# Optimization experiments

Hardware: AMD Instinct MI355X
Metric: run time of the kernel (lower is better)

The kernel has to match this reference:

```python
import jax, jax.numpy as jnp
import numpy as np

D_MODEL = 768
NHEAD = 12
HEAD_DIM = D_MODEL // NHEAD


def setup_inputs() -> dict:
    key = jax.random.key(0)
    ks = jax.random.split(key, 5)
    B, S = 1, 4096
    x = jax.random.normal(ks[0], (B, S, D_MODEL), dtype=jnp.float32)
    # Linear params (stored as [in, out] so y = x @ W + b)
    s_in = 1.0 / np.sqrt(D_MODEL)
    W_qkv = jax.random.uniform(ks[1], (D_MODEL, 3 * D_MODEL), minval=-s_in, maxval=s_in, dtype=jnp.float32)
    b_qkv = jax.random.uniform(ks[2], (3 * D_MODEL,), minval=-s_in, maxval=s_in, dtype=jnp.float32)
    W_o = jax.random.uniform(ks[3], (D_MODEL, D_MODEL), minval=-s_in, maxval=s_in, dtype=jnp.float32)
    b_o = jax.random.uniform(ks[4], (D_MODEL,), minval=-s_in, maxval=s_in, dtype=jnp.float32)
    return {"x": x, "W_qkv": W_qkv, "b_qkv": b_qkv, "W_o": W_o, "b_o": b_o}


def reference(x, W_qkv, b_qkv, W_o, b_o):
    B, S, _ = x.shape
    qkv = x @ W_qkv + b_qkv                      # [B,S,3D]
    qkv = qkv.reshape(B, S, 3, NHEAD, HEAD_DIM)
    q, k, v = qkv[:, :, 0], qkv[:, :, 1], qkv[:, :, 2]   # [B,S,H,hd]
    scale = D_MODEL ** (-0.5)                    # NOTE: d_model, not head_dim
    scores = jnp.einsum('bqhd,bkhd->bhqk', q, k) * scale
    attn = jax.nn.softmax(scores, axis=-1)
    out = jnp.einsum('bhqk,bkhd->bqhd', attn, v) * HEAD_DIM  # custom post-softmax rescale
    out = out.reshape(B, S, D_MODEL)
    return out @ W_o + b_o
```

## Files before the change

kernel.cpp:

```cpp
#include <hip/hip_runtime.h>
#include <stdint.h>
#include <math.h>

typedef unsigned short u16;
typedef __attribute__((ext_vector_type(8))) __bf16 bf16x8;
typedef __attribute__((ext_vector_type(4))) float f32x4;
typedef __attribute__((ext_vector_type(16))) float f32x16;
typedef __attribute__((ext_vector_type(4))) short short4v;
typedef __attribute__((ext_vector_type(4))) float float4v;
typedef __attribute__((ext_vector_type(2))) uint32_t u32x2;
typedef __attribute__((ext_vector_type(4))) uint32_t u32x4;

#define SEQ 4096
#define DM 768
#define NH 12

__device__ __forceinline__ u16 f2b(float f) {
  uint32_t u = __float_as_uint(f);
  uint32_t r = (u + 0x7fffu + ((u >> 16) & 1u)) >> 16;
  return (u16)r;
}

__device__ __forceinline__ uint32_t cvtpk(float lo, float hi) {
  uint32_t r;
  asm("v_cvt_pk_bf16_f32 %0, %1, %2" : "=v"(r) : "v"(lo), "v"(hi));
  return r;
}

__device__ __forceinline__ void gload16(const void* g, void* l) {
  __builtin_amdgcn_global_load_lds(
      (const __attribute__((address_space(1))) void*)g,
      (__attribute__((address_space(3))) void*)l, 16, 0, 0);
}

__device__ __forceinline__ f32x4 mfma16(bf16x8 a, bf16x8 b, f32x4 c) {
  return __builtin_amdgcn_mfma_f32_16x16x32_bf16(a, b, c, 0, 0, 0);
}

__device__ __forceinline__ f32x16 mfma32(bf16x8 a, bf16x8 b, f32x16 c) {
  return __builtin_amdgcn_mfma_f32_32x32x16_bf16(a, b, c, 0, 0, 0);
}

__device__ __forceinline__ float pexp2(float x) {
  return fmaf(fmaf(fmaf(0.0571709f, x, 0.249989f), x, 0.6927303f), x, 0.9987737f);
}

__global__ __launch_bounds__(256) void k_conv(const float* __restrict__ in,
                                              u16* __restrict__ out) {
  int i = blockIdx.x * 256 + threadIdx.x;
  float4v v = ((const float4v*)in)[i];
  short4v o;
  o.x = (short)f2b(v.x);
  o.y = (short)f2b(v.y);
  o.z = (short)f2b(v.z);
  o.w = (short)f2b(v.w);
  ((short4v*)out)[i] = o;
}

__global__ __launch_bounds__(256) void k_transconv(const float* __restrict__ in,
                                                   u16* __restrict__ out,
                                                   int R, int C) {
  __shared__ float tile[32][33];
  int tx = threadIdx.x & 31, ty = threadIdx.x >> 5;
  int r0 = blockIdx.y * 32, c0 = blockIdx.x * 32;
#pragma unroll
  for (int k = 0; k < 4; ++k)
    tile[ty + 8 * k][tx] = in[(size_t)(r0 + ty + 8 * k) * C + c0 + tx];
  __syncthreads();
#pragma unroll
  for (int k = 0; k < 4; ++k)
    out[(size_t)(c0 + ty + 8 * k) * R + r0 + tx] = f2b(tile[tx][ty + 8 * k]);
}

template <int EPI>
__global__ __launch_bounds__(256) void k_gemm(
    const u16* __restrict__ A, const u16* __restrict__ Bt,
    const float* __restrict__ bias, float* __restrict__ Cf,
    u16* __restrict__ qh, u16* __restrict__ kh, u16* __restrict__ vT,
    int M, int N, int K) {
  __shared__ u16 sA[128 * 64];
  __shared__ u16 sB[128 * 64];
  const int tid = threadIdx.x;
  const int w = tid >> 6, l = tid & 63;
  const int wr = w >> 1, wc = w & 1;
  const int lg = l >> 4, lc = l & 15;
  const int row0 = blockIdx.y * 128, col0 = blockIdx.x * 128;
  const int trg = tid >> 3;
  const int cg = ((tid & 7) ^ (trg & 7)) * 8;
  char* ldsA = (char*)sA + (w << 10);
  char* ldsB = (char*)sB + (w << 10);
  f32x4 acc[4][4] = {};
  for (int ks = 0; ks < K; ks += 64) {
#pragma unroll
    for (int i = 0; i < 4; ++i) {
      gload16(A + (size_t)(row0 + i * 32 + trg) * K + ks + cg, ldsA + i * 4096);
      gload16(Bt + (size_t)(col0 + i * 32 + trg) * K + ks + cg, ldsB + i * 4096);
    }
    __syncthreads();
#pragma unroll
    for (int kk = 0; kk < 2; ++kk) {
      bf16x8 af[4], bfr[4];
#pragma unroll
      for (int m = 0; m < 4; ++m)
        af[m] = *(const bf16x8*)&sA[(wr * 64 + m * 16 + lc) * 64 +
                                    (((kk << 2) + lg) ^ (lc & 7)) * 8];
#pragma unroll
      for (int n = 0; n < 4; ++n)
        bfr[n] = *(const bf16x8*)&sB[(wc * 64 + n * 16 + lc) * 64 +
                                     (((kk << 2) + lg) ^ (lc & 7)) * 8];
#pragma unroll
      for (int m = 0; m < 4; ++m)
#pragma unroll
        for (int n = 0; n < 4; ++n)
          acc[m][n] = mfma16(af[m], bfr[n], acc[m][n]);
    }
    __syncthreads();
  }
  const float QSC = 0.036084391824351615f * 1.4426950408889634f;
#pragma unroll
  for (int m = 0; m < 4; ++m) {
    const int grow0 = row0 + wr * 64 + m * 16 + lg * 4;
#pragma unroll
    for (int n = 0; n < 4; ++n) {
      const int gcol = col0 + wc * 64 + n * 16 + lc;
      const float bb = bias[gcol];
      if (EPI == 1) {
#pragma unroll
        for (int r = 0; r < 4; ++r)
          Cf[(size_t)(grow0 + r) * N + gcol] = acc[m][n][r] + bb;
      } else {
        const int typ = gcol / DM;
        const int hd = gcol % DM;
        const int h = hd >> 6, d = hd & 63;
        if (typ == 2) {
          u32x2 pk2;
          pk2.x = cvtpk(acc[m][n][0] + bb, acc[m][n][1] + bb);
          pk2.y = cvtpk(acc[m][n][2] + bb, acc[m][n][3] + bb);
          *(u32x2*)&vT[(size_t)(h * 64 + d) * SEQ + grow0] = pk2;
        } else if (typ == 0) {
#pragma unroll
          for (int r = 0; r < 4; ++r)
            qh[((size_t)h * SEQ + grow0 + r) * 64 + d] = f2b((acc[m][n][r] + bb) * QSC);
        } else {
          const int lgp = ((lg & 1) << 1) | (lg >> 1);
          const int growp = row0 + wr * 64 + m * 16 + lgp * 4;
#pragma unroll
          for (int r = 0; r < 4; ++r)
            kh[((size_t)h * SEQ + growp + r) * 64 + d] = f2b(acc[m][n][r] + bb);
        }
      }
    }
  }
}

__global__ __launch_bounds__(256) void k_gemm_s(
    const u16* __restrict__ A, const u16* __restrict__ Bt,
    const float* __restrict__ bias, float* __restrict__ Cf,
    int M, int N, int K) {
  __shared__ u16 sA[64 * 64];
  __shared__ u16 sB[64 * 64];
  const int tid = threadIdx.x;
  const int w = tid >> 6, l = tid & 63;
  const int wr = w >> 1, wc = w & 1;
  const int lg = l >> 4, lc = l & 15;
  const int row0 = blockIdx.y * 64, col0 = blockIdx.x * 64;
  const int trg = tid >> 3;
  const int cg = ((tid & 7) ^ (trg & 7)) * 8;
  char* ldsA = (char*)sA + (w << 10);
  char* ldsB = (char*)sB + (w << 10);
  f32x4 acc[2][2] = {};
  for (int ks = 0; ks < K; ks += 64) {
    gload16(A + (size_t)(row0 + trg) * K + ks + cg, ldsA);
    gload16(A + (size_t)(row0 + 32 + trg) * K + ks + cg, ldsA + 4096);
    gload16(Bt + (size_t)(col0 + trg) * K + ks + cg, ldsB);
    gload16(Bt + (size_t)(col0 + 32 + trg) * K + ks + cg, ldsB + 4096);
    __syncthreads();
#pragma unroll
    for (int kk = 0; kk < 2; ++kk) {
      bf16x8 af[2], bfr[2];
#pragma unroll
      for (int m = 0; m < 2; ++m)
        af[m] = *(const bf16x8*)&sA[(wr * 32 + m * 16 + lc) * 64 +
                                    (((kk << 2) + lg) ^ (lc & 7)) * 8];
#pragma unroll
      for (int n = 0; n < 2; ++n)
        bfr[n] = *(const bf16x8*)&sB[(wc * 32 + n * 16 + lc) * 64 +
                                     (((kk << 2) + lg) ^ (lc & 7)) * 8];
#pragma unroll
      for (int m = 0; m < 2; ++m)
#pragma unroll
        for (int n = 0; n < 2; ++n)
          acc[m][n] = mfma16(af[m], bfr[n], acc[m][n]);
    }
    __syncthreads();
  }
#pragma unroll
  for (int m = 0; m < 2; ++m) {
    const int grow0 = row0 + wr * 32 + m * 16 + lg * 4;
#pragma unroll
    for (int n = 0; n < 2; ++n) {
      const int gcol = col0 + wc * 32 + n * 16 + lc;
      const float bb = bias[gcol];
#pragma unroll
      for (int r = 0; r < 4; ++r)
        Cf[(size_t)(grow0 + r) * N + gcol] = acc[m][n][r] + bb;
    }
  }
}

__global__ __launch_bounds__(256, 3) void k_attn(
    const u16* __restrict__ qh, const u16* __restrict__ kh,
    const u16* __restrict__ vT, u16* __restrict__ att) {
  __shared__ alignas(16) u16 smem[5 * 4096];
  u16* const sQ = smem;
  u16* const sK0 = smem + 4096;
  u16* const sK1 = smem + 2 * 4096;
  u16* const sV0 = smem + 3 * 4096;
  u16* const sV1 = smem + 4 * 4096;
  const int tid = threadIdx.x;
  const int w = tid >> 6, l = tid & 63;
  const int l31 = l & 31, hi = l >> 5;
  const int khalf = w & 1, qhf = w >> 1;
  const int fid = blockIdx.x;
  const int swz = (fid & 7) * 96 + (fid >> 3);
  const int h = swz >> 6;
  const int q0 = (swz & 63) << 6;
  const int tr8 = tid >> 3;
  const int cc = ((tid & 7) ^ (tr8 & 7)) * 8;
  const u16* Qg = qh + ((size_t)h * SEQ + q0) * 64;
  const u16* Kg = kh + (size_t)h * SEQ * 64;
  const u16* Vg = vT + (size_t)h * 64 * SEQ;
  gload16(Qg + (size_t)tr8 * 64 + cc, (char*)sQ + (w << 10));
  gload16(Qg + (size_t)(32 + tr8) * 64 + cc, (char*)sQ + 4096 + (w << 10));
  gload16(Kg + (size_t)tr8 * 64 + cc, (char*)sK0 + (w << 10));
  gload16(Kg + (size_t)(32 + tr8) * 64 + cc, (char*)sK0 + 4096 + (w << 10));
  gload16(Vg + (size_t)tr8 * SEQ + cc, (char*)sV0 + (w << 10));
  gload16(Vg + (size_t)(32 + tr8) * SEQ + cc, (char*)sV0 + 4096 + (w << 10));
  __syncthreads();
  const int qrow = qhf * 32 + l31;
  const int krow = khalf * 32 + l31;
  bf16x8 qf[4];
#pragma unroll
  for (int ds = 0; ds < 4; ++ds)
    qf[ds] = *(const bf16x8*)&sQ[qrow * 64 + (((ds << 1) + hi) ^ (qrow & 7)) * 8];
  f32x16 oacc0 = {}, oacc1 = {};
  float l_r = 0.f;

  auto body = [&](const u16* sKc, const u16* sVc, char* nK, char* nV, int t) {
    if (t < 63) {
      const int k1 = (t + 1) * 64;
      gload16(Kg + (size_t)(k1 + tr8) * 64 + cc, nK + (w << 10));
      gload16(Kg + (size_t)(k1 + 32 + tr8) * 64 + cc, nK + 4096 + (w << 10));
      gload16(Vg + (size_t)tr8 * SEQ + k1 + cc, nV + (w << 10));
      gload16(Vg + (size_t)(32 + tr8) * SEQ + k1 + cc, nV + 4096 + (w << 10));
    }
    f32x16 sa = {};
    __builtin_amdgcn_s_setprio(1);
#pragma unroll
    for (int ds = 0; ds < 4; ++ds) {
      bf16x8 kf = *(const bf16x8*)&sKc[krow * 64 + (((ds << 1) + hi) ^ (krow & 7)) * 8];
      sa = mfma32(kf, qf[ds], sa);
    }
    __builtin_amdgcn_s_setprio(0);
    float p[16];
#pragma unroll
    for (int r = 0; r < 16; ++r) p[r] = pexp2(sa[r]);
    l_r += (((p[0] + p[1]) + (p[2] + p[3])) + ((p[4] + p[5]) + (p[6] + p[7]))) +
           (((p[8] + p[9]) + (p[10] + p[11])) + ((p[12] + p[13]) + (p[14] + p[15])));
    u32x4 w0v, w1v;
    w0v.x = cvtpk(p[0], p[1]);
    w0v.y = cvtpk(p[2], p[3]);
    w0v.z = cvtpk(p[4], p[5]);
    w0v.w = cvtpk(p[6], p[7]);
    w1v.x = cvtpk(p[8], p[9]);
    w1v.y = cvtpk(p[10], p[11]);
    w1v.z = cvtpk(p[12], p[13]);
    w1v.w = cvtpk(p[14], p[15]);
    const bf16x8 pf0 = __builtin_bit_cast(bf16x8, w0v);
    const bf16x8 pf1 = __builtin_bit_cast(bf16x8, w1v);
    __builtin_amdgcn_s_setprio(1);
    {
      const int vr0 = l31, vr1 = 32 + l31;
      bf16x8 v00 = *(const bf16x8*)&sVc[vr0 * 64 + (((khalf << 2) + 0 + hi) ^ (vr0 & 7)) * 8];
      bf16x8 v01 = *(const bf16x8*)&sVc[vr0 * 64 + (((khalf << 2) + 2 + hi) ^ (vr0 & 7)) * 8];
      oacc0 = mfma32(v00, pf0, oacc0);
      oacc0 = mfma32(v01, pf1, oacc0);
      bf16x8 v10 = *(const bf16x8*)&sVc[vr1 * 64 + (((khalf << 2) + 0 + hi) ^ (vr1 & 7)) * 8];
      bf16x8 v11 = *(const bf16x8*)&sVc[vr1 * 64 + (((khalf << 2) + 2 + hi) ^ (vr1 & 7)) * 8];
      oacc1 = mfma32(v10, pf0, oacc1);
      oacc1 = mfma32(v11, pf1, oacc1);
    }
    __builtin_amdgcn_s_setprio(0);
    __syncthreads();
  };

  for (int t = 0; t < 64; t += 2) {
    body(sK0, sV0, (char*)sK1, (char*)sV1, t);
    body(sK1, sV1, (char*)sK0, (char*)sV0, t + 1);
  }

  l_r += __shfl_xor(l_r, 32);
  float* xch = (float*)smem;
  float* mySlot = xch + (w * 64 + l) * 17;
  const f32x16 owrite = khalf ? oacc0 : oacc1;
#pragma unroll
  for (int r = 0; r < 16; ++r) mySlot[r] = owrite[r];
  mySlot[16] = l_r;
  __syncthreads();
  const float* pSlot = xch + (((w ^ 1) * 64) + l) * 17;
  f32x16 okeep = khalf ? oacc1 : oacc0;
  const float lt = l_r + pSlot[16];
#pragma unroll
  for (int r = 0; r < 16; ++r) okeep[r] += pSlot[r];
  const float li = 64.0f / lt;
  u16* orow = att + (size_t)(q0 + qrow) * DM + h * 64 + khalf * 32 + hi * 4;
#pragma unroll
  for (int g = 0; g < 4; ++g) {
    u32x2 pk2;
    pk2.x = cvtpk(okeep[4 * g + 0] * li, okeep[4 * g + 1] * li);
    pk2.y = cvtpk(okeep[4 * g + 2] * li, okeep[4 * g + 3] * li);
    *(u32x2*)(orow + 8 * g) = pk2;
  }
}

extern "C" void kernel_launch(void* const* d_in, const int* in_sizes, int n_in,
                              void* d_out, int out_size, void* d_ws, size_t ws_size,
                              hipStream_t stream) {
  const float* x = (const float*)d_in[0];
  const float* W_qkv = (const float*)d_in[1];
  const float* b_qkv = (const float*)d_in[2];
  const float* W_o = (const float*)d_in[3];
  const float* b_o = (const float*)d_in[4];
  float* out = (float*)d_out;
  char* ws = (char*)d_ws;
  u16* x_bf = (u16*)(ws);
  u16* wqkvT = (u16*)(ws + 6291456);
  u16* woT = (u16*)(ws + 9830400);
  u16* qh = (u16*)(ws + 11010048);
  u16* kh = (u16*)(ws + 17301504);
  u16* vT = (u16*)(ws + 23592960);
  u16* att = (u16*)(ws + 29884416);

  k_conv<<<dim3(3072), dim3(256), 0, stream>>>(x, x_bf);
  k_transconv<<<dim3(72, 24), dim3(256), 0, stream>>>(W_qkv, wqkvT, DM, 3 * DM);
  k_transconv<<<dim3(24, 24), dim3(256), 0, stream>>>(W_o, woT, DM, DM);
  k_gemm<0><<<dim3(18, 32), dim3(256), 0, stream>>>(
      x_bf, wqkvT, b_qkv, nullptr, qh, kh, vT, SEQ, 3 * DM, DM);
  k_attn<<<dim3(768), dim3(256), 0, stream>>>(qh, kh, vT, att);
  k_gemm_s<<<dim3(12, 64), dim3(256), 0, stream>>>(
      att, woT, b_o, out, SEQ, DM, DM);
}
```

Before: 119.8 us.

## Merge preprocessing kernels into one launch and retile QKV GEMM to 128x64

The three conversion and transpose kernels for x, W_qkv and W_o become a single launch, with each block picking its job from its block index. This removes two kernel launches and the gaps between them. The QKV projection GEMM now uses 128x64 tiles, so each block covers exactly one head of one of q, k or v. That doubles the block count from 576 to 1152 for better fill of the GPU's compute units and makes the epilogue branch the same for the whole block. The cost is less operand reuse per block, since A tiles are loaded twice as often.

```diff
diff --git a/kernel.cpp b/kernel.cpp
--- a/kernel.cpp
+++ b/kernel.cpp
@@ -45,24 +45,36 @@
   return fmaf(fmaf(fmaf(0.0571709f, x, 0.249989f), x, 0.6927303f), x, 0.9987737f);
 }
 
-__global__ __launch_bounds__(256) void k_conv(const float* __restrict__ in,
-                                              u16* __restrict__ out) {
-  int i = blockIdx.x * 256 + threadIdx.x;
-  float4v v = ((const float4v*)in)[i];
-  short4v o;
-  o.x = (short)f2b(v.x);
-  o.y = (short)f2b(v.y);
-  o.z = (short)f2b(v.z);
-  o.w = (short)f2b(v.w);
-  ((short4v*)out)[i] = o;
-}
-
-__global__ __launch_bounds__(256) void k_transconv(const float* __restrict__ in,
-                                                   u16* __restrict__ out,
-                                                   int R, int C) {
+__global__ __launch_bounds__(256) void k_pre(
+    const float* __restrict__ x, u16* __restrict__ x_bf,
+    const float* __restrict__ Wq, u16* __restrict__ wqT,
+    const float* __restrict__ Wo, u16* __restrict__ woT) {
   __shared__ float tile[32][33];
-  int tx = threadIdx.x & 31, ty = threadIdx.x >> 5;
-  int r0 = blockIdx.y * 32, c0 = blockIdx.x * 32;
+  const int bid = blockIdx.x;
+  const int tid = threadIdx.x;
+  if (bid < 3072) {
+    int i = bid * 256 + tid;
+    float4v v = ((const float4v*)x)[i];
+    short4v o;
+    o.x = (short)f2b(v.x);
+    o.y = (short)f2b(v.y);
+    o.z = (short)f2b(v.z);
+    o.w = (short)f2b(v.w);
+    ((short4v*)x_bf)[i] = o;
+    return;
+  }
+  const float* in;
+  u16* out;
+  int R, C, bx, by;
+  if (bid < 4800) {
+    in = Wq; out = wqT; R = DM; C = 3 * DM;
+    bx = (bid - 3072) % 72; by = (bid - 3072) / 72;
+  } else {
+    in = Wo; out = woT; R = DM; C = DM;
+    bx = (bid - 4800) % 24; by = (bid - 4800) / 24;
+  }
+  int tx = tid & 31, ty = tid >> 5;
+  int r0 = by * 32, c0 = bx * 32;
 #pragma unroll
   for (int k = 0; k < 4; ++k)
     tile[ty + 8 * k][tx] = in[(size_t)(r0 + ty + 8 * k) * C + c0 + tx];
@@ -72,44 +84,42 @@
     out[(size_t)(c0 + ty + 8 * k) * R + r0 + tx] = f2b(tile[tx][ty + 8 * k]);
 }
 
-template <int EPI>
-__global__ __launch_bounds__(256) void k_gemm(
+__global__ __launch_bounds__(256) void k_gemm_qkv(
     const u16* __restrict__ A, const u16* __restrict__ Bt,
-    const float* __restrict__ bias, float* __restrict__ Cf,
-    u16* __restrict__ qh, u16* __restrict__ kh, u16* __restrict__ vT,
-    int M, int N, int K) {
+    const float* __restrict__ bias,
+    u16* __restrict__ qh, u16* __restrict__ kh, u16* __restrict__ vT) {
   __shared__ u16 sA[128 * 64];
-  __shared__ u16 sB[128 * 64];
+  __shared__ u16 sB[64 * 64];
   const int tid = threadIdx.x;
   const int w = tid >> 6, l = tid & 63;
-  const int wr = w >> 1, wc = w & 1;
   const int lg = l >> 4, lc = l & 15;
-  const int row0 = blockIdx.y * 128, col0 = blockIdx.x * 128;
+  const int row0 = blockIdx.y * 128, col0 = blockIdx.x * 64;
   const int trg = tid >> 3;
   const int cg = ((tid & 7) ^ (trg & 7)) * 8;
   char* ldsA = (char*)sA + (w << 10);
   char* ldsB = (char*)sB + (w << 10);
-  f32x4 acc[4][4] = {};
-  for (int ks = 0; ks < K; ks += 64) {
-#pragma unroll
-    for (int i = 0; i < 4; ++i) {
-      gload16(A + (size_t)(row0 + i * 32 + trg) * K + ks + cg, ldsA + i * 4096);
-      gload16(Bt + (size_t)(col0 + i * 32 + trg) * K + ks + cg, ldsB + i * 4096);
-    }
+  f32x4 acc[2][4] = {};
+  for (int ks = 0; ks < DM; ks += 64) {
+#pragma unroll
+    for (int i = 0; i < 4; ++i)
+      gload16(A + (size_t)(row0 + i * 32 + trg) * DM + ks + cg, ldsA + i * 4096);
+#pragma unroll
+    for (int i = 0; i < 2; ++i)
+      gload16(Bt + (size_t)(col0 + i * 32 + trg) * DM + ks + cg, ldsB + i * 4096);
     __syncthreads();
 #pragma unroll
     for (int kk = 0; kk < 2; ++kk) {
-      bf16x8 af[4], bfr[4];
-#pragma unroll
-      for (int m = 0; m < 4; ++m)
-        af[m] = *(const bf16x8*)&sA[(wr * 64 + m * 16 + lc) * 64 +
+      bf16x8 af[2], bfr[4];
+#pragma unroll
+      for (int m = 0; m < 2; ++m)
+        af[m] = *(const bf16x8*)&sA[(w * 32 + m * 16 + lc) * 64 +
                                     (((kk << 2) + lg) ^ (lc & 7)) * 8];
 #pragma unroll
       for (int n = 0; n < 4; ++n)
-        bfr[n] = *(const bf16x8*)&sB[(wc * 64 + n * 16 + lc) * 64 +
+        bfr[n] = *(const bf16x8*)&sB[(n * 16 + lc) * 64 +
                                      (((kk << 2) + lg) ^ (lc & 7)) * 8];
 #pragma unroll
-      for (int m = 0; m < 4; ++m)
+      for (int m = 0; m < 2; ++m)
 #pragma unroll
         for (int n = 0; n < 4; ++n)
           acc[m][n] = mfma16(af[m], bfr[n], acc[m][n]);
@@ -117,37 +127,30 @@
     __syncthreads();
   }
   const float QSC = 0.036084391824351615f * 1.4426950408889634f;
-#pragma unroll
-  for (int m = 0; m < 4; ++m) {
-    const int grow0 = row0 + wr * 64 + m * 16 + lg * 4;
+  const int typ = col0 / DM;
+  const int h = (col0 % DM) >> 6;
+#pragma unroll
+  for (int m = 0; m < 2; ++m) {
+    const int grow0 = row0 + w * 32 + m * 16 + lg * 4;
 #pragma unroll
     for (int n = 0; n < 4; ++n) {
-      const int gcol = col0 + wc * 64 + n * 16 + lc;
-      const float bb = bias[gcol];
-      if (EPI == 1) {
+      const int d = n * 16 + lc;
+      const float bb = bias[col0 + d];
+      if (typ == 2) {
+        u32x2 pk2;
+        pk2.x = cvtpk(acc[m][n][0] + bb, acc[m][n][1] + bb);
+        pk2.y = cvtpk(acc[m][n][2] + bb, acc[m][n][3] + bb);
+        *(u32x2*)&vT[(size_t)(h * 64 + d) * SEQ + grow0] = pk2;
+      } else if (typ == 0) {
 #pragma unroll
         for (int r = 0; r < 4; ++r)
-          Cf[(size_t)(grow0 + r) * N + gcol] = acc[m][n][r] + bb;
+          qh[((size_t)h * SEQ + grow0 + r) * 64 + d] = f2b((acc[m][n][r] + bb) * QSC);
       } else {
-        const int typ = gcol / DM;
-        const int hd = gcol % DM;
-        const int h = hd >> 6, d = hd & 63;
-        if (typ == 2) {
-          u32x2 pk2;
-          pk2.x = cvtpk(acc[m][n][0] + bb, acc[m][n][1] + bb);
-          pk2.y = cvtpk(acc[m][n][2] + bb, acc[m][n][3] + bb);
-          *(u32x2*)&vT[(size_t)(h * 64 + d) * SEQ + grow0] = pk2;
-        } else if (typ == 0) {
-#pragma unroll
-          for (int r = 0; r < 4; ++r)
-            qh[((size_t)h * SEQ + grow0 + r) * 64 + d] = f2b((acc[m][n][r] + bb) * QSC);
-        } else {
-          const int lgp = ((lg & 1) << 1) | (lg >> 1);
-          const int growp = row0 + wr * 64 + m * 16 + lgp * 4;
-#pragma unroll
-          for (int r = 0; r < 4; ++r)
-            kh[((size_t)h * SEQ + growp + r) * 64 + d] = f2b(acc[m][n][r] + bb);
-        }
+        const int lgp = ((lg & 1) << 1) | (lg >> 1);
+        const int growp = row0 + w * 32 + m * 16 + lgp * 4;
+#pragma unroll
+        for (int r = 0; r < 4; ++r)
+          kh[((size_t)h * SEQ + growp + r) * 64 + d] = f2b(acc[m][n][r] + bb);
       }
     }
   }
@@ -341,11 +344,9 @@
   u16* vT = (u16*)(ws + 23592960);
   u16* att = (u16*)(ws + 29884416);
 
-  k_conv<<<dim3(3072), dim3(256), 0, stream>>>(x, x_bf);
-  k_transconv<<<dim3(72, 24), dim3(256), 0, stream>>>(W_qkv, wqkvT, DM, 3 * DM);
-  k_transconv<<<dim3(24, 24), dim3(256), 0, stream>>>(W_o, woT, DM, DM);
-  k_gemm<0><<<dim3(18, 32), dim3(256), 0, stream>>>(
-      x_bf, wqkvT, b_qkv, nullptr, qh, kh, vT, SEQ, 3 * DM, DM);
+  k_pre<<<dim3(5376), dim3(256), 0, stream>>>(x, x_bf, W_qkv, wqkvT, W_o, woT);
+  k_gemm_qkv<<<dim3(36, 32), dim3(256), 0, stream>>>(
+      x_bf, wqkvT, b_qkv, qh, kh, vT);
   k_attn<<<dim3(768), dim3(256), 0, stream>>>(qh, kh, vT, att);
   k_gemm_s<<<dim3(12, 64), dim3(256), 0, stream>>>(
       att, woT, b_o, out, SEQ, DM, DM);
```

After: 114.8 us. -4.2%, faster.
